# Kernel tuning notes

Hardware: AMD Instinct MI355X
Metric: run time of the kernel (lower is better)

Reference implementation:

```python
import jax, jax.numpy as jnp
import numpy as np

B, N, DIM = 2, 4096, 1024
HEADS, HEAD_DIM, CHUNK, LAYERS, HID = 16, 64, 128, 4, 4096
SCALE = HEAD_DIM ** -0.5
EPS = 1e-6


def _bitlinear(x, w, b):
    # BitLinear 1.58b: ternary weights + int8 activations with STE
    w_scale = jnp.maximum(jnp.mean(jnp.abs(w)), 1e-5)
    w_norm = w / w_scale
    w_q = w_norm + jax.lax.stop_gradient(jnp.sign(w_norm) - w_norm)
    x_scale = jnp.maximum(jnp.max(jnp.abs(x), axis=-1, keepdims=True), 1e-5)
    x_norm = x / x_scale * 127.0
    x_q = x_norm + jax.lax.stop_gradient(jnp.round(x_norm) - x_norm)
    out = (x_q @ w_q.T) * (x_scale * w_scale / 127.0)
    return out + b


def _rmsnorm(x, w):
    return x * jax.lax.rsqrt(jnp.mean(x * x, axis=-1, keepdims=True) + EPS) * w


def _rope_tables(n, d):
    inv = 1.0 / (10000.0 ** (jnp.arange(0, d, 2, dtype=jnp.float32) / d))
    f = jnp.arange(n, dtype=jnp.float32)[:, None] * inv[None, :]  # (N, d/2)
    return jnp.cos(f), jnp.sin(f)


def _apply_rope(x, cos, sin):
    # x: (B,N,H,D); complex pairs are consecutive last-dim elements
    xr, xi = x[..., 0::2], x[..., 1::2]
    c = cos[None, :, None, :]
    s = sin[None, :, None, :]
    or_ = xr * c - xi * s
    oi_ = xr * s + xi * c
    return jnp.stack([or_, oi_], axis=-1).reshape(x.shape)


def _attention(x, qkv_w, qkv_b, gate_w, gate_b, proj_w, proj_b, norm_w, cos, sin):
    b, n, c = x.shape
    qkv = _bitlinear(x, qkv_w, qkv_b).reshape(b, n, 3, HEADS, HEAD_DIM)
    q, k, v = qkv[:, :, 0], qkv[:, :, 1], qkv[:, :, 2]
    q = _apply_rope(q, cos, sin)
    k = _apply_rope(k, cos, sin)
    g = jax.nn.sigmoid(_bitlinear(x, gate_w, gate_b)).reshape(b, n, HEADS, HEAD_DIM)
    nc = n // CHUNK  # N is a multiple of CHUNK, so no padding

    def chunked(t):  # (B,N,H,D) -> (nc,B,L,H,D)
        return t.reshape(b, nc, CHUNK, HEADS, HEAD_DIM).transpose(1, 0, 2, 3, 4)

    def step(kv, inp):
        qi, ki, vi, gi = inp  # (B,L,H,D)
        # NOTE: faithful to source — attention mixes over the HEAD axis per position
        attn = jax.nn.softmax(jnp.einsum('blhd,blgd->blhg', qi, ki) * SCALE, axis=-1)
        out = jnp.einsum('blhg,blgd->blhd', attn, vi) + jnp.einsum('blhd,bhde->blhe', qi, kv)
        decay = jnp.mean(gi, axis=1)[..., None]  # (B,H,D,1)
        kv = kv * decay + jnp.einsum('blhd,blhe->bhde', ki, vi)
        return kv, out

    kv0 = jnp.zeros((b, HEADS, HEAD_DIM, HEAD_DIM), x.dtype)
    _, outs = jax.lax.scan(step, kv0, (chunked(q), chunked(k), chunked(v), chunked(g)))
    out = outs.transpose(1, 0, 2, 3, 4).reshape(b, n, c)
    return _bitlinear(_rmsnorm(out, norm_w), proj_w, proj_b)


def _mlp(x, fc1_w, fc1_b, fc2_w, fc2_b):
    h = _bitlinear(x, fc1_w, fc1_b)
    a, gate = jnp.split(h, 2, axis=-1)
    return _bitlinear(a * jax.nn.silu(gate), fc2_w, fc2_b)


def setup_inputs() -> dict:
    key = jax.random.key(0)
    ks = jax.random.split(key, 12)
    s = 0.02
    return {
        'x': jax.random.normal(ks[0], (B, N, DIM), jnp.float32),
        'norm1_w': jnp.ones((LAYERS, DIM), jnp.float32),
        'qkv_w': s * jax.random.normal(ks[1], (LAYERS, 3 * DIM, DIM), jnp.float32),
        'qkv_b': 0.01 * jax.random.normal(ks[2], (LAYERS, 3 * DIM), jnp.float32),
        'gate_w': s * jax.random.normal(ks[3], (LAYERS, DIM, DIM), jnp.float32),
        'gate_b': 0.01 * jax.random.normal(ks[4], (LAYERS, DIM), jnp.float32),
        'proj_w': s * jax.random.normal(ks[5], (LAYERS, DIM, DIM), jnp.float32),
        'proj_b': 0.01 * jax.random.normal(ks[6], (LAYERS, DIM), jnp.float32),
        'attn_norm_w': jnp.ones((LAYERS, DIM), jnp.float32),
        'norm2_w': jnp.ones((LAYERS, DIM), jnp.float32),
        'fc1_w': s * jax.random.normal(ks[7], (LAYERS, 2 * HID, DIM), jnp.float32),
        'fc1_b': 0.01 * jax.random.normal(ks[8], (LAYERS, 2 * HID), jnp.float32),
        'fc2_w': s * jax.random.normal(ks[9], (LAYERS, DIM, HID), jnp.float32),
        'fc2_b': 0.01 * jax.random.normal(ks[10], (LAYERS, DIM), jnp.float32),
    }


def reference(x, norm1_w, qkv_w, qkv_b, gate_w, gate_b, proj_w, proj_b,
              attn_norm_w, norm2_w, fc1_w, fc1_b, fc2_w, fc2_b):
    cos, sin = _rope_tables(x.shape[1], HEAD_DIM)
    for l in range(norm1_w.shape[0]):
        x = x + _attention(_rmsnorm(x, norm1_w[l]), qkv_w[l], qkv_b[l], gate_w[l],
                           gate_b[l], proj_w[l], proj_b[l], attn_norm_w[l], cos, sin)
        x = x + _mlp(_rmsnorm(x, norm2_w[l]), fc1_w[l], fc1_b[l], fc2_w[l], fc2_b[l])
    return x
```

## Files before the change

kernel.cpp:

```cpp
#include <hip/hip_runtime.h>
#include <hip/hip_bf16.h>
#include <cstdint>
#include <cstddef>

#define NLAYERS 4
#define SEQ     4096
#define DIMC    1024
#define CHUNKL  128
#define NCHUNK  32
#define HIDF    4096
#define NTOK    8192

using i32x4 = __attribute__((ext_vector_type(4))) int;

__device__ __forceinline__ void gload16(const void* g, void* l) {
    __builtin_amdgcn_global_load_lds((const __attribute__((address_space(1))) void*)g,
                                     (__attribute__((address_space(3))) void*)l, 16, 0, 0);
}

__device__ __forceinline__ float waveSum(float v) {
#pragma unroll
    for (int o = 32; o >= 1; o >>= 1) v += __shfl_down(v, o);
    return v;
}
__device__ __forceinline__ float waveMax(float v) {
#pragma unroll
    for (int o = 32; o >= 1; o >>= 1) v = fmaxf(v, __shfl_down(v, o));
    return v;
}

__global__ __launch_bounds__(256) void prep_k(const float* __restrict__ w, int8_t* __restrict__ q,
                                              float* __restrict__ part, int perlayer4) {
    __shared__ float red[4];
    int blk = blockIdx.x, layer = blockIdx.y, tid = threadIdx.x;
    const float4* p = (const float4*)(w + (size_t)layer * perlayer4 * 4);
    char4* qp = (char4*)(q + (size_t)layer * perlayer4 * 4);
    float s = 0.f;
    for (int i = blk * 256 + tid; i < perlayer4; i += 256 * 256) {
        float4 v = p[i];
        s += fabsf(v.x) + fabsf(v.y) + fabsf(v.z) + fabsf(v.w);
        char4 o;
        o.x = (v.x > 0.f) ? 1 : ((v.x < 0.f) ? -1 : 0);
        o.y = (v.y > 0.f) ? 1 : ((v.y < 0.f) ? -1 : 0);
        o.z = (v.z > 0.f) ? 1 : ((v.z < 0.f) ? -1 : 0);
        o.w = (v.w > 0.f) ? 1 : ((v.w < 0.f) ? -1 : 0);
        qp[i] = o;
    }
    s = waveSum(s);
    int lane = tid & 63, wv = tid >> 6;
    if (lane == 0) red[wv] = s;
    __syncthreads();
    if (tid == 0) part[layer * 256 + blk] = red[0] + red[1] + red[2] + red[3];
}

__global__ __launch_bounds__(256) void amean_fin(const float* __restrict__ part,
                                                 float* __restrict__ wsc, int perlayer) {
    __shared__ float red[4];
    int layer = blockIdx.x, tid = threadIdx.x;
    float s = part[layer * 256 + tid];
    s = waveSum(s);
    int lane = tid & 63, wv = tid >> 6;
    if (lane == 0) red[wv] = s;
    __syncthreads();
    if (tid == 0) {
        float tot = red[0] + red[1] + red[2] + red[3];
        wsc[layer] = fmaxf(tot / (float)perlayer, 1e-5f);
    }
}

__global__ __launch_bounds__(256) void ropetab_k(float* __restrict__ ct, float* __restrict__ st) {
    int i = blockIdx.x * 256 + threadIdx.x;
    int n = i >> 5, j = i & 31;
    float inv = exp2f(-(float)j * (13.287712379549449f / 32.0f));
    float f = (float)n * inv;
    ct[i] = cosf(f);
    st[i] = sinf(f);
}

__device__ __forceinline__ float4 rope4(float4 v, const float* ct, const float* st, int n, int j0) {
    float c0 = ct[n * 32 + j0], s0 = st[n * 32 + j0];
    float c1 = ct[n * 32 + j0 + 1], s1 = st[n * 32 + j0 + 1];
    float4 r;
    r.x = v.x * c0 - v.y * s0;
    r.y = v.x * s0 + v.y * c0;
    r.z = v.z * c1 - v.w * s1;
    r.w = v.z * s1 + v.w * c1;
    return r;
}

__global__ __launch_bounds__(256) void rmsq_k(const float* __restrict__ x, const float* __restrict__ w,
                                              int8_t* __restrict__ xq, float* __restrict__ xs) {
    __shared__ float red[4];
    int row = blockIdx.x, tid = threadIdx.x;
    const float4* xr = (const float4*)(x + (size_t)row * DIMC);
    float4 v = xr[tid];
    float ss = v.x * v.x + v.y * v.y + v.z * v.z + v.w * v.w;
    ss = waveSum(ss);
    int lane = tid & 63, wv = tid >> 6;
    if (lane == 0) red[wv] = ss;
    __syncthreads();
    float tot = red[0] + red[1] + red[2] + red[3];
    __syncthreads();
    float rinv = 1.0f / sqrtf(tot * (1.0f / (float)DIMC) + 1e-6f);
    float4 wv4 = ((const float4*)w)[tid];
    float4 y;
    y.x = v.x * rinv * wv4.x; y.y = v.y * rinv * wv4.y;
    y.z = v.z * rinv * wv4.z; y.w = v.w * rinv * wv4.w;
    float mx = fmaxf(fmaxf(fabsf(y.x), fabsf(y.y)), fmaxf(fabsf(y.z), fabsf(y.w)));
    mx = waveMax(mx);
    if (lane == 0) red[wv] = mx;
    __syncthreads();
    float s = fmaxf(fmaxf(fmaxf(red[0], red[1]), fmaxf(red[2], red[3])), 1e-5f);
    if (tid == 0) xs[row] = s;
    float qf = 127.0f / s;
    char4 o;
    o.x = (signed char)(int)rintf(y.x * qf);
    o.y = (signed char)(int)rintf(y.y * qf);
    o.z = (signed char)(int)rintf(y.z * qf);
    o.w = (signed char)(int)rintf(y.w * qf);
    ((char4*)xq)[(size_t)row * 256 + tid] = o;
}

__global__ __launch_bounds__(256) void qrow_k(const float* __restrict__ in,
                                              int8_t* __restrict__ q, float* __restrict__ xs) {
    __shared__ float red[4];
    int row = blockIdx.x, tid = threadIdx.x;
    const float4* xr = (const float4*)(in + (size_t)row * HIDF);
    float4 vv[4];
    float mx = 0.f;
#pragma unroll
    for (int j = 0; j < 4; ++j) {
        vv[j] = xr[j * 256 + tid];
        mx = fmaxf(mx, fmaxf(fmaxf(fabsf(vv[j].x), fabsf(vv[j].y)), fmaxf(fabsf(vv[j].z), fabsf(vv[j].w))));
    }
    mx = waveMax(mx);
    int lane = tid & 63, wv = tid >> 6;
    if (lane == 0) red[wv] = mx;
    __syncthreads();
    float s = fmaxf(fmaxf(fmaxf(red[0], red[1]), fmaxf(red[2], red[3])), 1e-5f);
    if (tid == 0) xs[row] = s;
    float qf = 127.0f / s;
#pragma unroll
    for (int j = 0; j < 4; ++j) {
        char4 o;
        o.x = (signed char)(int)rintf(vv[j].x * qf);
        o.y = (signed char)(int)rintf(vv[j].y * qf);
        o.z = (signed char)(int)rintf(vv[j].z * qf);
        o.w = (signed char)(int)rintf(vv[j].w * qf);
        ((char4*)q)[(size_t)row * 1024 + j * 256 + tid] = o;
    }
}

#define EPI_PLAIN 0
#define EPI_RESID 2

template <int EPI>
__global__ __launch_bounds__(256, 4) void gemm_i8(const int8_t* __restrict__ A,
                                                  const int8_t* __restrict__ B,
                                                  const float* __restrict__ xs,
                                                  const float* __restrict__ wsp,
                                                  const float* __restrict__ bias,
                                                  float* __restrict__ out,
                                                  int N, int K, int ldo) {
    __shared__ __align__(16) int8_t As[16384];
    __shared__ __align__(16) int8_t Bs[16384];
    const int tid = threadIdx.x;
    const int lane = tid & 63, wave = tid >> 6;
    const int wr = wave >> 1, wc = wave & 1;
    const int bm = blockIdx.x, bn = blockIdx.y;

    const int rA = tid >> 3;
    const int colb = (((tid & 7) ^ (rA & 7)) << 4);
    const int8_t* ap = A + (size_t)(bm * 128 + rA) * K + colb;
    const int8_t* bp = B + (size_t)(bn * 128 + rA) * K + colb;
    const size_t rstep = (size_t)32 * K;

    i32x4 acc[4][4] = {};
    const int fr = lane & 15, ks = lane >> 4;

    for (int kt = 0; kt < K; kt += 128) {
#pragma unroll
        for (int p = 0; p < 4; ++p) {
            gload16(ap + kt + (size_t)p * rstep, As + p * 4096 + tid * 16);
            gload16(bp + kt + (size_t)p * rstep, Bs + p * 4096 + tid * 16);
        }
        __syncthreads();
#pragma unroll
        for (int kh = 0; kh < 2; ++kh) {
            i32x4 af[4], bf[4];
#pragma unroll
            for (int m = 0; m < 4; ++m) {
                int ra = wr * 64 + m * 16 + fr;
                af[m] = *(const i32x4*)(As + ra * 128 + (((kh * 4 + ks) ^ (ra & 7)) << 4));
            }
#pragma unroll
            for (int n = 0; n < 4; ++n) {
                int rb = wc * 64 + n * 16 + fr;
                bf[n] = *(const i32x4*)(Bs + rb * 128 + (((kh * 4 + ks) ^ (rb & 7)) << 4));
            }
#pragma unroll
            for (int m = 0; m < 4; ++m)
#pragma unroll
                for (int n = 0; n < 4; ++n)
                    acc[m][n] = __builtin_amdgcn_mfma_i32_16x16x64_i8(af[m], bf[n], acc[m][n], 0, 0, 0);
        }
        __syncthreads();
    }

    const float ws = *wsp;
#pragma unroll
    for (int m = 0; m < 4; ++m) {
        int row0 = bm * 128 + wr * 64 + m * 16 + ks * 4;
#pragma unroll
        for (int n = 0; n < 4; ++n) {
            int col = bn * 128 + wc * 64 + n * 16 + fr;
            float bv = bias[col];
#pragma unroll
            for (int j = 0; j < 4; ++j) {
                int row = row0 + j;
                float v = (float)acc[m][n][j] * (xs[row] * ws * (1.0f / 127.0f)) + bv;
                size_t idx = (size_t)row * ldo + col;
                if (EPI == EPI_PLAIN) out[idx] = v;
                else                  out[idx] += v;
            }
        }
    }
    (void)N;
}

__global__ __launch_bounds__(256, 4) void gate_decay(const int8_t* __restrict__ A,
                                                     const int8_t* __restrict__ B,
                                                     const float* __restrict__ xs,
                                                     const float* __restrict__ wsp,
                                                     const float* __restrict__ bias,
                                                     float* __restrict__ dec) {
    __shared__ __align__(16) int8_t As[16384];
    __shared__ __align__(16) int8_t Bs[16384];
    __shared__ float dsum[2][128];
    const int tid = threadIdx.x;
    const int lane = tid & 63, wave = tid >> 6;
    const int wr = wave >> 1, wc = wave & 1;
    const int bm = blockIdx.x, bn = blockIdx.y;
    const int K = 1024;

    const int rA = tid >> 3;
    const int colb = (((tid & 7) ^ (rA & 7)) << 4);
    const int8_t* ap = A + (size_t)(bm * 128 + rA) * K + colb;
    const int8_t* bp = B + (size_t)(bn * 128 + rA) * K + colb;
    const size_t rstep = (size_t)32 * K;

    i32x4 acc[4][4] = {};
    const int fr = lane & 15, ks = lane >> 4;

    for (int kt = 0; kt < K; kt += 128) {
#pragma unroll
        for (int p = 0; p < 4; ++p) {
            gload16(ap + kt + (size_t)p * rstep, As + p * 4096 + tid * 16);
            gload16(bp + kt + (size_t)p * rstep, Bs + p * 4096 + tid * 16);
        }
        __syncthreads();
#pragma unroll
        for (int kh = 0; kh < 2; ++kh) {
            i32x4 af[4], bf[4];
#pragma unroll
            for (int m = 0; m < 4; ++m) {
                int ra = wr * 64 + m * 16 + fr;
                af[m] = *(const i32x4*)(As + ra * 128 + (((kh * 4 + ks) ^ (ra & 7)) << 4));
            }
#pragma unroll
            for (int n = 0; n < 4; ++n) {
                int rb = wc * 64 + n * 16 + fr;
                bf[n] = *(const i32x4*)(Bs + rb * 128 + (((kh * 4 + ks) ^ (rb & 7)) << 4));
            }
#pragma unroll
            for (int m = 0; m < 4; ++m)
#pragma unroll
                for (int n = 0; n < 4; ++n)
                    acc[m][n] = __builtin_amdgcn_mfma_i32_16x16x64_i8(af[m], bf[n], acc[m][n], 0, 0, 0);
        }
        __syncthreads();
    }

    const float ws = *wsp;
#pragma unroll
    for (int n = 0; n < 4; ++n) {
        int col = bn * 128 + wc * 64 + n * 16 + fr;
        float bv = bias[col];
        float sn = 0.f;
#pragma unroll
        for (int m = 0; m < 4; ++m) {
            int row0 = bm * 128 + wr * 64 + m * 16 + ks * 4;
#pragma unroll
            for (int j = 0; j < 4; ++j) {
                int row = row0 + j;
                float v = (float)acc[m][n][j] * (xs[row] * ws * (1.0f / 127.0f)) + bv;
                sn += 1.0f / (1.0f + expf(-v));
            }
        }
        sn += __shfl_down(sn, 32);
        sn += __shfl_down(sn, 16);
        if (lane < 16) dsum[wr][wc * 64 + n * 16 + lane] = sn;
    }
    __syncthreads();
    if (tid < 128) {
        int b = bm >> 5, c = bm & 31;
        dec[(size_t)(c * 2 + b) * 1024 + bn * 128 + tid] =
            (dsum[0][tid] + dsum[1][tid]) * (1.0f / 128.0f);
    }
}

__global__ __launch_bounds__(256, 4) void gemm_fc1(const int8_t* __restrict__ A,
                                                   const int8_t* __restrict__ B1,
                                                   const int8_t* __restrict__ B2,
                                                   const float* __restrict__ xs,
                                                   const float* __restrict__ wsp,
                                                   const float* __restrict__ bias,
                                                   float* __restrict__ out) {
    __shared__ __align__(16) int8_t As[16384];
    __shared__ __align__(16) int8_t Bs1[8192];
    __shared__ __align__(16) int8_t Bs2[8192];
    const int tid = threadIdx.x;
    const int lane = tid & 63, wave = tid >> 6;
    const int wr = wave >> 1, wc = wave & 1;
    const int bm = blockIdx.x, bn = blockIdx.y;
    const int K = 1024;

    const int rA = tid >> 3;
    const int colb = (((tid & 7) ^ (rA & 7)) << 4);
    const int8_t* ap  = A  + (size_t)(bm * 128 + rA) * K + colb;
    const int8_t* b1p = B1 + (size_t)(bn * 64 + rA) * K + colb;
    const int8_t* b2p = B2 + (size_t)(bn * 64 + rA) * K + colb;
    const size_t rstep = (size_t)32 * K;

    i32x4 acc1[4][2] = {}, acc2[4][2] = {};
    const int fr = lane & 15, ks = lane >> 4;

    for (int kt = 0; kt < K; kt += 128) {
#pragma unroll
        for (int p = 0; p < 4; ++p)
            gload16(ap + kt + (size_t)p * rstep, As + p * 4096 + tid * 16);
#pragma unroll
        for (int p = 0; p < 2; ++p) {
            gload16(b1p + kt + (size_t)p * rstep, Bs1 + p * 4096 + tid * 16);
            gload16(b2p + kt + (size_t)p * rstep, Bs2 + p * 4096 + tid * 16);
        }
        __syncthreads();
#pragma unroll
        for (int kh = 0; kh < 2; ++kh) {
            i32x4 af[4], b1f[2], b2f[2];
#pragma unroll
            for (int m = 0; m < 4; ++m) {
                int ra = wr * 64 + m * 16 + fr;
                af[m] = *(const i32x4*)(As + ra * 128 + (((kh * 4 + ks) ^ (ra & 7)) << 4));
            }
#pragma unroll
            for (int n = 0; n < 2; ++n) {
                int rb = wc * 32 + n * 16 + fr;
                int off = rb * 128 + (((kh * 4 + ks) ^ (rb & 7)) << 4);
                b1f[n] = *(const i32x4*)(Bs1 + off);
                b2f[n] = *(const i32x4*)(Bs2 + off);
            }
#pragma unroll
            for (int m = 0; m < 4; ++m)
#pragma unroll
                for (int n = 0; n < 2; ++n) {
                    acc1[m][n] = __builtin_amdgcn_mfma_i32_16x16x64_i8(af[m], b1f[n], acc1[m][n], 0, 0, 0);
                    acc2[m][n] = __builtin_amdgcn_mfma_i32_16x16x64_i8(af[m], b2f[n], acc2[m][n], 0, 0, 0);
                }
        }
        __syncthreads();
    }

    const float ws = *wsp;
#pragma unroll
    for (int m = 0; m < 4; ++m) {
        int row0 = bm * 128 + wr * 64 + m * 16 + ks * 4;
#pragma unroll
        for (int n = 0; n < 2; ++n) {
            int col = bn * 64 + wc * 32 + n * 16 + fr;
            float ba = bias[col];
            float bg = bias[col + 4096];
#pragma unroll
            for (int j = 0; j < 4; ++j) {
                int row = row0 + j;
                float sc = xs[row] * ws * (1.0f / 127.0f);
                float a = (float)acc1[m][n][j] * sc + ba;
                float g = (float)acc2[m][n][j] * sc + bg;
                out[(size_t)row * HIDF + col] = a * g / (1.0f + expf(-g));
            }
        }
    }
}

__global__ __launch_bounds__(256) void attn_intra(const float* __restrict__ qkv,
                                                  const float* __restrict__ ct,
                                                  const float* __restrict__ st,
                                                  float* __restrict__ o) {
    __shared__ float q_s[1024], k_s[1024], v_s[1024], p_s[256];
    int t = blockIdx.x, tid = threadIdx.x;
    int n = t & (SEQ - 1);
    int j0 = (tid & 15) * 2;
    const float4* src = (const float4*)(qkv + (size_t)t * 3072);
    ((float4*)q_s)[tid] = rope4(src[tid], ct, st, n, j0);
    ((float4*)k_s)[tid] = rope4(src[256 + tid], ct, st, n, j0);
    ((float4*)v_s)[tid] = src[512 + tid];
    __syncthreads();
    int h = tid >> 4, g = tid & 15;
    const float4* q4 = (const float4*)q_s + h * 16;
    const float4* k4 = (const float4*)k_s + g * 16;
    float accS = 0.f;
#pragma unroll
    for (int i = 0; i < 16; ++i) {
        float4 qa = q4[i], ka = k4[i];
        accS += qa.x * ka.x + qa.y * ka.y + qa.z * ka.z + qa.w * ka.w;
    }
    accS *= 0.125f;
    float mx = accS;
#pragma unroll
    for (int o2 = 8; o2 >= 1; o2 >>= 1) mx = fmaxf(mx, __shfl_xor(mx, o2, 16));
    float e = expf(accS - mx);
    float sm = e;
#pragma unroll
    for (int o2 = 8; o2 >= 1; o2 >>= 1) sm += __shfl_xor(sm, o2, 16);
    p_s[tid] = e / sm;
    __syncthreads();
    int dq = tid & 15;
    float4 acc = {0.f, 0.f, 0.f, 0.f};
    const float4* v4 = (const float4*)v_s;
#pragma unroll
    for (int gg = 0; gg < 16; ++gg) {
        float p = p_s[h * 16 + gg];
        float4 vv = v4[gg * 16 + dq];
        acc.x += p * vv.x; acc.y += p * vv.y; acc.z += p * vv.z; acc.w += p * vv.w;
    }
    ((float4*)(o + (size_t)t * DIMC))[h * 16 + dq] = acc;
}

__global__ __launch_bounds__(256) void u_k(const float* __restrict__ qkv,
                                           const float* __restrict__ ct,
                                           const float* __restrict__ st,
                                           float* __restrict__ U) {
    __shared__ float ks_[8192], vs_[8192];
    int bid = blockIdx.x, tid = threadIdx.x;
    int c = bid >> 5, b = (bid >> 4) & 1, h = bid & 15;
    size_t tok = (size_t)(b * SEQ + c * CHUNKL);
#pragma unroll
    for (int j = 0; j < 8; ++j) {
        int idx = j * 256 + tid;
        int l = idx >> 4, c4 = idx & 15;
        int n = (int)((tok + l) & (SEQ - 1));
        const float* kp = qkv + (tok + l) * 3072 + 1024 + h * 64 + c4 * 4;
        const float* vp = qkv + (tok + l) * 3072 + 2048 + h * 64 + c4 * 4;
        ((float4*)ks_)[idx] = rope4(*(const float4*)kp, ct, st, n, c4 * 2);
        ((float4*)vs_)[idx] = *(const float4*)vp;
    }
    __syncthreads();
    int d = tid >> 2, eg = tid & 3;
    float4 acc[4] = {};
    for (int l = 0; l < CHUNKL; ++l) {
        float kd = ks_[l * 64 + d];
        const float4* vrow = (const float4*)(vs_ + l * 64) + eg * 4;
#pragma unroll
        for (int i = 0; i < 4; ++i) {
            float4 vv = vrow[i];
            acc[i].x += kd * vv.x; acc[i].y += kd * vv.y;
            acc[i].z += kd * vv.z; acc[i].w += kd * vv.w;
        }
    }
    float4* Up = (float4*)(U + (size_t)bid * 4096) + d * 16 + eg * 4;
#pragma unroll
    for (int i = 0; i < 4; ++i) Up[i] = acc[i];
}

__global__ __launch_bounds__(256) void scan_k(const float* __restrict__ U,
                                              const float* __restrict__ dec,
                                              float* __restrict__ kvprev) {
    int t = blockIdx.x * 256 + threadIdx.x;
    int b = t >> 16;
    int h = (t >> 12) & 15;
    int d = (t >> 6) & 63;
    float val = 0.f;
#pragma unroll 1
    for (int c = 0; c < NCHUNK; ++c) {
        kvprev[(size_t)c * 131072 + t] = val;
        val = val * dec[(c * 2 + b) * 1024 + h * 64 + d] + U[(size_t)c * 131072 + t];
    }
}

__global__ __launch_bounds__(256) void out2_k(const float* __restrict__ qkv,
                                              const float* __restrict__ ct,
                                              const float* __restrict__ st,
                                              const float* __restrict__ kvprev,
                                              float* __restrict__ o) {
    __shared__ float kv_s[4096];
    __shared__ float q_s[128 * 65];
    int bid = blockIdx.x, tid = threadIdx.x;
    int c = bid >> 5, b = (bid >> 4) & 1, h = bid & 15;
    size_t tok = (size_t)(b * SEQ + c * CHUNKL);
    const float4* kvsrc = (const float4*)(kvprev + (size_t)c * 131072 + b * 65536 + h * 4096);
#pragma unroll
    for (int j = 0; j < 4; ++j) ((float4*)kv_s)[j * 256 + tid] = kvsrc[j * 256 + tid];
#pragma unroll
    for (int j = 0; j < 8; ++j) {
        int idx = j * 256 + tid;
        int l = idx >> 4, c4 = idx & 15;
        int n = (int)((tok + l) & (SEQ - 1));
        float4 qv = rope4(*(const float4*)(qkv + (tok + l) * 3072 + h * 64 + c4 * 4),
                          ct, st, n, c4 * 2);
        float* dq = q_s + l * 65 + c4 * 4;
        dq[0] = qv.x; dq[1] = qv.y; dq[2] = qv.z; dq[3] = qv.w;
    }
    __syncthreads();
    int l = tid >> 1, eh = tid & 1;
    float4 acc[8] = {};
    const float* qrow = q_s + l * 65;
    for (int d = 0; d < 64; ++d) {
        float qd = qrow[d];
        const float4* kvr = (const float4*)(kv_s + d * 64) + eh * 8;
#pragma unroll
        for (int i = 0; i < 8; ++i) {
            float4 kk = kvr[i];
            acc[i].x += qd * kk.x; acc[i].y += qd * kk.y;
            acc[i].z += qd * kk.z; acc[i].w += qd * kk.w;
        }
    }
    float4* op = (float4*)(o + (tok + l) * DIMC + h * 64 + eh * 32);
#pragma unroll
    for (int i = 0; i < 8; ++i) {
        float4 cur = op[i];
        cur.x += acc[i].x; cur.y += acc[i].y; cur.z += acc[i].z; cur.w += acc[i].w;
        op[i] = cur;
    }
}

extern "C" void kernel_launch(void* const* d_in, const int* in_sizes, int n_in,
                              void* d_out, int out_size, void* d_ws, size_t ws_size,
                              hipStream_t stream) {
    const float* x_in       = (const float*)d_in[0];
    const float* norm1_w    = (const float*)d_in[1];
    const float* qkv_w      = (const float*)d_in[2];
    const float* qkv_b      = (const float*)d_in[3];
    const float* gate_w     = (const float*)d_in[4];
    const float* gate_b     = (const float*)d_in[5];
    const float* proj_w     = (const float*)d_in[6];
    const float* proj_b     = (const float*)d_in[7];
    const float* attn_norm_w= (const float*)d_in[8];
    const float* norm2_w    = (const float*)d_in[9];
    const float* fc1_w      = (const float*)d_in[10];
    const float* fc1_b      = (const float*)d_in[11];
    const float* fc2_w      = (const float*)d_in[12];
    const float* fc2_b      = (const float*)d_in[13];
    float* x = (float*)d_out;

    char* wsb = (char*)d_ws;
    size_t off = 0;
    auto carve = [&](size_t bytes) { char* p = wsb + off; off = (off + bytes + 255) & ~(size_t)255; return p; };
    int8_t* q_qkv  = (int8_t*)carve(12582912);
    int8_t* q_gate = (int8_t*)carve(4194304);
    int8_t* q_proj = (int8_t*)carve(4194304);
    int8_t* q_fc1  = (int8_t*)carve(33554432);
    int8_t* q_fc2  = (int8_t*)carve(16777216);
    float*  wsc    = (float*)carve(256);
    float*  part   = (float*)carve(4096);
    float*  ropec  = (float*)carve(524288);
    float*  ropes  = (float*)carve(524288);
    int8_t* qbuf   = (int8_t*)carve(33554432);
    float*  xsbuf  = (float*)carve(32768);
    float*  big    = (float*)carve(134217728);
    float*  attn_o = (float*)carve(33554432);
    float*  Ub     = (float*)carve(16777216);
    float*  kvprev = (float*)carve(16777216);
    float*  decayb = (float*)carve(262144);
    (void)ws_size; (void)in_sizes; (void)n_in; (void)out_size;

    hipMemcpyAsync(x, x_in, (size_t)NTOK * DIMC * sizeof(float), hipMemcpyDeviceToDevice, stream);
    ropetab_k<<<512, 256, 0, stream>>>(ropec, ropes);

    struct WSpec { const float* w; int8_t* q; int perlayer; int arr; };
    WSpec specs[5] = {
        {qkv_w,  q_qkv,  3 * DIMC * DIMC, 0},
        {gate_w, q_gate, DIMC * DIMC,     1},
        {proj_w, q_proj, DIMC * DIMC,     2},
        {fc1_w,  q_fc1,  8192 * 1024,     3},
        {fc2_w,  q_fc2,  DIMC * HIDF,     4},
    };
    for (int a = 0; a < 5; ++a) {
        prep_k<<<dim3(256, NLAYERS), 256, 0, stream>>>(specs[a].w, specs[a].q, part, specs[a].perlayer / 4);
        amean_fin<<<NLAYERS, 256, 0, stream>>>(part, wsc + specs[a].arr * 4, specs[a].perlayer);
    }

    for (int l = 0; l < NLAYERS; ++l) {
        rmsq_k<<<NTOK, 256, 0, stream>>>(x, norm1_w + l * DIMC, qbuf, xsbuf);
        gemm_i8<EPI_PLAIN><<<dim3(64, 24), 256, 0, stream>>>(
            qbuf, q_qkv + (size_t)l * 3145728, xsbuf, wsc + 0 * 4 + l,
            qkv_b + l * 3072, big, 3072, 1024, 3072);
        gate_decay<<<dim3(64, 8), 256, 0, stream>>>(
            qbuf, q_gate + (size_t)l * 1048576, xsbuf, wsc + 1 * 4 + l,
            gate_b + l * DIMC, decayb);
        attn_intra<<<NTOK, 256, 0, stream>>>(big, ropec, ropes, attn_o);
        u_k<<<1024, 256, 0, stream>>>(big, ropec, ropes, Ub);
        scan_k<<<512, 256, 0, stream>>>(Ub, decayb, kvprev);
        out2_k<<<1024, 256, 0, stream>>>(big, ropec, ropes, kvprev, attn_o);
        rmsq_k<<<NTOK, 256, 0, stream>>>(attn_o, attn_norm_w + l * DIMC, qbuf, xsbuf);
        gemm_i8<EPI_RESID><<<dim3(64, 8), 256, 0, stream>>>(
            qbuf, q_proj + (size_t)l * 1048576, xsbuf, wsc + 2 * 4 + l,
            proj_b + l * DIMC, x, 1024, 1024, 1024);
        rmsq_k<<<NTOK, 256, 0, stream>>>(x, norm2_w + l * DIMC, qbuf, xsbuf);
        gemm_fc1<<<dim3(64, 64), 256, 0, stream>>>(
            qbuf, q_fc1 + (size_t)l * 8388608, q_fc1 + (size_t)l * 8388608 + 4194304,
            xsbuf, wsc + 3 * 4 + l, fc1_b + l * 8192, big);
        qrow_k<<<NTOK, 256, 0, stream>>>(big, qbuf, xsbuf);
        gemm_i8<EPI_RESID><<<dim3(64, 8), 256, 0, stream>>>(
            qbuf, q_fc2 + (size_t)l * 4194304, xsbuf, wsc + 4 * 4 + l,
            fc2_b + l * DIMC, x, 1024, 4096, 1024);
    }
}
```

Before: 2.008 ms.

## Double-buffer LDS tiles in int8 GEMMs to overlap loads with MFMA

Converts the three int8 MFMA GEMM kernels from a single 128-wide K tile (load, sync, compute, sync) to a double-buffered 64-wide K tile. The next tile's global->LDS loads are issued before computing on the current buffer, so memory latency can overlap with matrix math. The XOR swizzle is adjusted for 64-byte rows. It keeps the same LDS footprint but takes twice as many loop iterations, and so twice as many barriers per K. It also relies on the barrier at the end of each iteration to make the async LDS loads visible.

```diff
diff --git a/kernel.cpp b/kernel.cpp
--- a/kernel.cpp
+++ b/kernel.cpp
@@ -162,49 +162,56 @@
                                                   const float* __restrict__ bias,
                                                   float* __restrict__ out,
                                                   int N, int K, int ldo) {
-    __shared__ __align__(16) int8_t As[16384];
-    __shared__ __align__(16) int8_t Bs[16384];
+    __shared__ __align__(16) int8_t As[2][8192];
+    __shared__ __align__(16) int8_t Bs[2][8192];
     const int tid = threadIdx.x;
     const int lane = tid & 63, wave = tid >> 6;
     const int wr = wave >> 1, wc = wave & 1;
     const int bm = blockIdx.x, bn = blockIdx.y;
 
-    const int rA = tid >> 3;
-    const int colb = (((tid & 7) ^ (rA & 7)) << 4);
-    const int8_t* ap = A + (size_t)(bm * 128 + rA) * K + colb;
-    const int8_t* bp = B + (size_t)(bn * 128 + rA) * K + colb;
-    const size_t rstep = (size_t)32 * K;
+    const int r0 = tid >> 2, sl = tid & 3;
+    const int c0 = ((sl ^ ((r0 >> 1) & 3)) << 4);
+    const int r1 = r0 + 64;
+    const int8_t* a0 = A + (size_t)(bm * 128 + r0) * K + c0;
+    const int8_t* a1 = A + (size_t)(bm * 128 + r1) * K + c0;
+    const int8_t* b0 = B + (size_t)(bn * 128 + r0) * K + c0;
+    const int8_t* b1 = B + (size_t)(bn * 128 + r1) * K + c0;
 
     i32x4 acc[4][4] = {};
     const int fr = lane & 15, ks = lane >> 4;
 
-    for (int kt = 0; kt < K; kt += 128) {
-#pragma unroll
-        for (int p = 0; p < 4; ++p) {
-            gload16(ap + kt + (size_t)p * rstep, As + p * 4096 + tid * 16);
-            gload16(bp + kt + (size_t)p * rstep, Bs + p * 4096 + tid * 16);
-        }
+    gload16(a0, As[0] + tid * 16);
+    gload16(a1, As[0] + 4096 + tid * 16);
+    gload16(b0, Bs[0] + tid * 16);
+    gload16(b1, Bs[0] + 4096 + tid * 16);
+    __syncthreads();
+
+    int cur = 0;
+    for (int kt = 0; kt < K; kt += 64) {
+        if (kt + 64 < K) {
+            gload16(a0 + kt + 64, As[cur ^ 1] + tid * 16);
+            gload16(a1 + kt + 64, As[cur ^ 1] + 4096 + tid * 16);
+            gload16(b0 + kt + 64, Bs[cur ^ 1] + tid * 16);
+            gload16(b1 + kt + 64, Bs[cur ^ 1] + 4096 + tid * 16);
+        }
+        i32x4 af[4], bf[4];
+#pragma unroll
+        for (int m = 0; m < 4; ++m) {
+            int ra = wr * 64 + m * 16 + fr;
+            af[m] = *(const i32x4*)(As[cur] + ra * 64 + ((ks ^ ((ra >> 1) & 3)) << 4));
+        }
+#pragma unroll
+        for (int n = 0; n < 4; ++n) {
+            int rb = wc * 64 + n * 16 + fr;
+            bf[n] = *(const i32x4*)(Bs[cur] + rb * 64 + ((ks ^ ((rb >> 1) & 3)) << 4));
+        }
+#pragma unroll
+        for (int m = 0; m < 4; ++m)
+#pragma unroll
+            for (int n = 0; n < 4; ++n)
+                acc[m][n] = __builtin_amdgcn_mfma_i32_16x16x64_i8(af[m], bf[n], acc[m][n], 0, 0, 0);
         __syncthreads();
-#pragma unroll
-        for (int kh = 0; kh < 2; ++kh) {
-            i32x4 af[4], bf[4];
-#pragma unroll
-            for (int m = 0; m < 4; ++m) {
-                int ra = wr * 64 + m * 16 + fr;
-                af[m] = *(const i32x4*)(As + ra * 128 + (((kh * 4 + ks) ^ (ra & 7)) << 4));
-            }
-#pragma unroll
-            for (int n = 0; n < 4; ++n) {
-                int rb = wc * 64 + n * 16 + fr;
-                bf[n] = *(const i32x4*)(Bs + rb * 128 + (((kh * 4 + ks) ^ (rb & 7)) << 4));
-            }
-#pragma unroll
-            for (int m = 0; m < 4; ++m)
-#pragma unroll
-                for (int n = 0; n < 4; ++n)
-                    acc[m][n] = __builtin_amdgcn_mfma_i32_16x16x64_i8(af[m], bf[n], acc[m][n], 0, 0, 0);
-        }
-        __syncthreads();
+        cur ^= 1;
     }
 
     const float ws = *wsp;
@@ -234,8 +241,8 @@
                                                      const float* __restrict__ wsp,
                                                      const float* __restrict__ bias,
                                                      float* __restrict__ dec) {
-    __shared__ __align__(16) int8_t As[16384];
-    __shared__ __align__(16) int8_t Bs[16384];
+    __shared__ __align__(16) int8_t As[2][8192];
+    __shared__ __align__(16) int8_t Bs[2][8192];
     __shared__ float dsum[2][128];
     const int tid = threadIdx.x;
     const int lane = tid & 63, wave = tid >> 6;
@@ -243,42 +250,49 @@
     const int bm = blockIdx.x, bn = blockIdx.y;
     const int K = 1024;
 
-    const int rA = tid >> 3;
-    const int colb = (((tid & 7) ^ (rA & 7)) << 4);
-    const int8_t* ap = A + (size_t)(bm * 128 + rA) * K + colb;
-    const int8_t* bp = B + (size_t)(bn * 128 + rA) * K + colb;
-    const size_t rstep = (size_t)32 * K;
+    const int r0 = tid >> 2, sl = tid & 3;
+    const int c0 = ((sl ^ ((r0 >> 1) & 3)) << 4);
+    const int r1 = r0 + 64;
+    const int8_t* a0 = A + (size_t)(bm * 128 + r0) * K + c0;
+    const int8_t* a1 = A + (size_t)(bm * 128 + r1) * K + c0;
+    const int8_t* b0 = B + (size_t)(bn * 128 + r0) * K + c0;
+    const int8_t* b1 = B + (size_t)(bn * 128 + r1) * K + c0;
 
     i32x4 acc[4][4] = {};
     const int fr = lane & 15, ks = lane >> 4;
 
-    for (int kt = 0; kt < K; kt += 128) {
-#pragma unroll
-        for (int p = 0; p < 4; ++p) {
-            gload16(ap + kt + (size_t)p * rstep, As + p * 4096 + tid * 16);
-            gload16(bp + kt + (size_t)p * rstep, Bs + p * 4096 + tid * 16);
-        }
+    gload16(a0, As[0] + tid * 16);
+    gload16(a1, As[0] + 4096 + tid * 16);
+    gload16(b0, Bs[0] + tid * 16);
+    gload16(b1, Bs[0] + 4096 + tid * 16);
+    __syncthreads();
+
+    int cur = 0;
+    for (int kt = 0; kt < K; kt += 64) {
+        if (kt + 64 < K) {
+            gload16(a0 + kt + 64, As[cur ^ 1] + tid * 16);
+            gload16(a1 + kt + 64, As[cur ^ 1] + 4096 + tid * 16);
+            gload16(b0 + kt + 64, Bs[cur ^ 1] + tid * 16);
+            gload16(b1 + kt + 64, Bs[cur ^ 1] + 4096 + tid * 16);
+        }
+        i32x4 af[4], bf[4];
+#pragma unroll
+        for (int m = 0; m < 4; ++m) {
+            int ra = wr * 64 + m * 16 + fr;
+            af[m] = *(const i32x4*)(As[cur] + ra * 64 + ((ks ^ ((ra >> 1) & 3)) << 4));
+        }
+#pragma unroll
+        for (int n = 0; n < 4; ++n) {
+            int rb = wc * 64 + n * 16 + fr;
+            bf[n] = *(const i32x4*)(Bs[cur] + rb * 64 + ((ks ^ ((rb >> 1) & 3)) << 4));
+        }
+#pragma unroll
+        for (int m = 0; m < 4; ++m)
+#pragma unroll
+            for (int n = 0; n < 4; ++n)
+                acc[m][n] = __builtin_amdgcn_mfma_i32_16x16x64_i8(af[m], bf[n], acc[m][n], 0, 0, 0);
         __syncthreads();
-#pragma unroll
-        for (int kh = 0; kh < 2; ++kh) {
-            i32x4 af[4], bf[4];
-#pragma unroll
-            for (int m = 0; m < 4; ++m) {
-                int ra = wr * 64 + m * 16 + fr;
-                af[m] = *(const i32x4*)(As + ra * 128 + (((kh * 4 + ks) ^ (ra & 7)) << 4));
-            }
-#pragma unroll
-            for (int n = 0; n < 4; ++n) {
-                int rb = wc * 64 + n * 16 + fr;
-                bf[n] = *(const i32x4*)(Bs + rb * 128 + (((kh * 4 + ks) ^ (rb & 7)) << 4));
-            }
-#pragma unroll
-            for (int m = 0; m < 4; ++m)
-#pragma unroll
-                for (int n = 0; n < 4; ++n)
-                    acc[m][n] = __builtin_amdgcn_mfma_i32_16x16x64_i8(af[m], bf[n], acc[m][n], 0, 0, 0);
-        }
-        __syncthreads();
+        cur ^= 1;
     }
 
     const float ws = *wsp;
@@ -316,59 +330,62 @@
                                                    const float* __restrict__ wsp,
                                                    const float* __restrict__ bias,
                                                    float* __restrict__ out) {
-    __shared__ __align__(16) int8_t As[16384];
-    __shared__ __align__(16) int8_t Bs1[8192];
-    __shared__ __align__(16) int8_t Bs2[8192];
+    __shared__ __align__(16) int8_t As[2][8192];
+    __shared__ __align__(16) int8_t Bs1[2][4096];
+    __shared__ __align__(16) int8_t Bs2[2][4096];
     const int tid = threadIdx.x;
     const int lane = tid & 63, wave = tid >> 6;
     const int wr = wave >> 1, wc = wave & 1;
     const int bm = blockIdx.x, bn = blockIdx.y;
     const int K = 1024;
 
-    const int rA = tid >> 3;
-    const int colb = (((tid & 7) ^ (rA & 7)) << 4);
-    const int8_t* ap  = A  + (size_t)(bm * 128 + rA) * K + colb;
-    const int8_t* b1p = B1 + (size_t)(bn * 64 + rA) * K + colb;
-    const int8_t* b2p = B2 + (size_t)(bn * 64 + rA) * K + colb;
-    const size_t rstep = (size_t)32 * K;
+    const int r0 = tid >> 2, sl = tid & 3;
+    const int c0 = ((sl ^ ((r0 >> 1) & 3)) << 4);
+    const int r1 = r0 + 64;
+    const int8_t* a0  = A  + (size_t)(bm * 128 + r0) * K + c0;
+    const int8_t* a1  = A  + (size_t)(bm * 128 + r1) * K + c0;
+    const int8_t* b1p = B1 + (size_t)(bn * 64 + r0) * K + c0;
+    const int8_t* b2p = B2 + (size_t)(bn * 64 + r0) * K + c0;
 
     i32x4 acc1[4][2] = {}, acc2[4][2] = {};
     const int fr = lane & 15, ks = lane >> 4;
 
-    for (int kt = 0; kt < K; kt += 128) {
-#pragma unroll
-        for (int p = 0; p < 4; ++p)
-            gload16(ap + kt + (size_t)p * rstep, As + p * 4096 + tid * 16);
-#pragma unroll
-        for (int p = 0; p < 2; ++p) {
-            gload16(b1p + kt + (size_t)p * rstep, Bs1 + p * 4096 + tid * 16);
-            gload16(b2p + kt + (size_t)p * rstep, Bs2 + p * 4096 + tid * 16);
-        }
+    gload16(a0,  As[0] + tid * 16);
+    gload16(a1,  As[0] + 4096 + tid * 16);
+    gload16(b1p, Bs1[0] + tid * 16);
+    gload16(b2p, Bs2[0] + tid * 16);
+    __syncthreads();
+
+    int cur = 0;
+    for (int kt = 0; kt < K; kt += 64) {
+        if (kt + 64 < K) {
+            gload16(a0  + kt + 64, As[cur ^ 1] + tid * 16);
+            gload16(a1  + kt + 64, As[cur ^ 1] + 4096 + tid * 16);
+            gload16(b1p + kt + 64, Bs1[cur ^ 1] + tid * 16);
+            gload16(b2p + kt + 64, Bs2[cur ^ 1] + tid * 16);
+        }
+        i32x4 af[4], b1f[2], b2f[2];
+#pragma unroll
+        for (int m = 0; m < 4; ++m) {
+            int ra = wr * 64 + m * 16 + fr;
+            af[m] = *(const i32x4*)(As[cur] + ra * 64 + ((ks ^ ((ra >> 1) & 3)) << 4));
+        }
+#pragma unroll
+        for (int n = 0; n < 2; ++n) {
+            int rb = wc * 32 + n * 16 + fr;
+            int off = rb * 64 + ((ks ^ ((rb >> 1) & 3)) << 4);
+            b1f[n] = *(const i32x4*)(Bs1[cur] + off);
+            b2f[n] = *(const i32x4*)(Bs2[cur] + off);
+        }
+#pragma unroll
+        for (int m = 0; m < 4; ++m)
+#pragma unroll
+            for (int n = 0; n < 2; ++n) {
+                acc1[m][n] = __builtin_amdgcn_mfma_i32_16x16x64_i8(af[m], b1f[n], acc1[m][n], 0, 0, 0);
+                acc2[m][n] = __builtin_amdgcn_mfma_i32_16x16x64_i8(af[m], b2f[n], acc2[m][n], 0, 0, 0);
+            }
         __syncthreads();
-#pragma unroll
-        for (int kh = 0; kh < 2; ++kh) {
-            i32x4 af[4], b1f[2], b2f[2];
-#pragma unroll
-            for (int m = 0; m < 4; ++m) {
-                int ra = wr * 64 + m * 16 + fr;
-                af[m] = *(const i32x4*)(As + ra * 128 + (((kh * 4 + ks) ^ (ra & 7)) << 4));
-            }
-#pragma unroll
-            for (int n = 0; n < 2; ++n) {
-                int rb = wc * 32 + n * 16 + fr;
-                int off = rb * 128 + (((kh * 4 + ks) ^ (rb & 7)) << 4);
-                b1f[n] = *(const i32x4*)(Bs1 + off);
-                b2f[n] = *(const i32x4*)(Bs2 + off);
-            }
-#pragma unroll
-            for (int m = 0; m < 4; ++m)
-#pragma unroll
-                for (int n = 0; n < 2; ++n) {
-                    acc1[m][n] = __builtin_amdgcn_mfma_i32_16x16x64_i8(af[m], b1f[n], acc1[m][n], 0, 0, 0);
-                    acc2[m][n] = __builtin_amdgcn_mfma_i32_16x16x64_i8(af[m], b2f[n], acc2[m][n], 0, 0, 0);
-                }
-        }
-        __syncthreads();
+        cur ^= 1;
     }
 
     const float ws = *wsp;
```

New measurement: 2.146 ms. 6.9% more time.

## Double-buffer fc1 int8 GEMM K-loop with async LDS prefetch

Applied to the files above, without the earlier changes.

Restructures the gated fc1 int8 GEMM main loop into a two-stage pipeline. K tiles shrink from 128 to 64 and are double-buffered in LDS, with the load for tile t+2 issued right after the current tile's fragments are read into registers. Explicit vmcnt/lgkmcnt waits and raw barriers replace the full __syncthreads pairs. The goal is to hide global-to-LDS load latency behind the MFMA work. In exchange the loop runs twice as many iterations with smaller tiles, and the swizzle changes to fit 64-byte rows.

```diff
diff --git a/kernel.cpp b/kernel.cpp
--- a/kernel.cpp
+++ b/kernel.cpp
@@ -316,60 +316,68 @@
                                                    const float* __restrict__ wsp,
                                                    const float* __restrict__ bias,
                                                    float* __restrict__ out) {
-    __shared__ __align__(16) int8_t As[16384];
-    __shared__ __align__(16) int8_t Bs1[8192];
-    __shared__ __align__(16) int8_t Bs2[8192];
+    __shared__ __align__(16) int8_t As[2][8192];
+    __shared__ __align__(16) int8_t Bs1[2][4096];
+    __shared__ __align__(16) int8_t Bs2[2][4096];
     const int tid = threadIdx.x;
     const int lane = tid & 63, wave = tid >> 6;
     const int wr = wave >> 1, wc = wave & 1;
     const int bm = blockIdx.x, bn = blockIdx.y;
     const int K = 1024;
 
-    const int rA = tid >> 3;
-    const int colb = (((tid & 7) ^ (rA & 7)) << 4);
-    const int8_t* ap  = A  + (size_t)(bm * 128 + rA) * K + colb;
-    const int8_t* b1p = B1 + (size_t)(bn * 64 + rA) * K + colb;
-    const int8_t* b2p = B2 + (size_t)(bn * 64 + rA) * K + colb;
-    const size_t rstep = (size_t)32 * K;
+    const int r0 = tid >> 2, sl = tid & 3;
+    const int c0 = ((sl ^ ((r0 >> 1) & 3)) << 4);
+    const int r1 = r0 + 64;
+    const int8_t* a0  = A  + (size_t)(bm * 128 + r0) * K + c0;
+    const int8_t* a1  = A  + (size_t)(bm * 128 + r1) * K + c0;
+    const int8_t* b1p = B1 + (size_t)(bn * 64 + r0) * K + c0;
+    const int8_t* b2p = B2 + (size_t)(bn * 64 + r0) * K + c0;
 
     i32x4 acc1[4][2] = {}, acc2[4][2] = {};
     const int fr = lane & 15, ks = lane >> 4;
 
-    for (int kt = 0; kt < K; kt += 128) {
-#pragma unroll
-        for (int p = 0; p < 4; ++p)
-            gload16(ap + kt + (size_t)p * rstep, As + p * 4096 + tid * 16);
-#pragma unroll
-        for (int p = 0; p < 2; ++p) {
-            gload16(b1p + kt + (size_t)p * rstep, Bs1 + p * 4096 + tid * 16);
-            gload16(b2p + kt + (size_t)p * rstep, Bs2 + p * 4096 + tid * 16);
-        }
-        __syncthreads();
-#pragma unroll
-        for (int kh = 0; kh < 2; ++kh) {
-            i32x4 af[4], b1f[2], b2f[2];
-#pragma unroll
-            for (int m = 0; m < 4; ++m) {
-                int ra = wr * 64 + m * 16 + fr;
-                af[m] = *(const i32x4*)(As + ra * 128 + (((kh * 4 + ks) ^ (ra & 7)) << 4));
-            }
+#define STAGE_FC1(buf, kt_)  do {                         \
+        gload16(a0  + (kt_), As[buf] + tid * 16);         \
+        gload16(a1  + (kt_), As[buf] + 4096 + tid * 16);  \
+        gload16(b1p + (kt_), Bs1[buf] + tid * 16);        \
+        gload16(b2p + (kt_), Bs2[buf] + tid * 16);        \
+    } while (0)
+
+    STAGE_FC1(0, 0);
+    STAGE_FC1(1, 64);
+
+    const int NT = 16;
+    for (int t = 0; t < NT; ++t) {
+        const int cur = t & 1;
+        if (t < NT - 1) asm volatile("s_waitcnt vmcnt(4)" ::: "memory");
+        else            asm volatile("s_waitcnt vmcnt(0)" ::: "memory");
+        __builtin_amdgcn_s_barrier();
+        i32x4 af[4], b1f[2], b2f[2];
+#pragma unroll
+        for (int m = 0; m < 4; ++m) {
+            int ra = wr * 64 + m * 16 + fr;
+            af[m] = *(const i32x4*)(As[cur] + ra * 64 + ((ks ^ ((ra >> 1) & 3)) << 4));
+        }
+#pragma unroll
+        for (int n = 0; n < 2; ++n) {
+            int rb = wc * 32 + n * 16 + fr;
+            int off = rb * 64 + ((ks ^ ((rb >> 1) & 3)) << 4);
+            b1f[n] = *(const i32x4*)(Bs1[cur] + off);
+            b2f[n] = *(const i32x4*)(Bs2[cur] + off);
+        }
+        asm volatile("s_waitcnt lgkmcnt(0)" ::: "memory");
+        __builtin_amdgcn_s_barrier();
+        __builtin_amdgcn_sched_barrier(0);
+        if (t + 2 < NT) STAGE_FC1(cur, (t + 2) * 64);
+#pragma unroll
+        for (int m = 0; m < 4; ++m)
 #pragma unroll
             for (int n = 0; n < 2; ++n) {
-                int rb = wc * 32 + n * 16 + fr;
-                int off = rb * 128 + (((kh * 4 + ks) ^ (rb & 7)) << 4);
-                b1f[n] = *(const i32x4*)(Bs1 + off);
-                b2f[n] = *(const i32x4*)(Bs2 + off);
-            }
-#pragma unroll
-            for (int m = 0; m < 4; ++m)
-#pragma unroll
-                for (int n = 0; n < 2; ++n) {
-                    acc1[m][n] = __builtin_amdgcn_mfma_i32_16x16x64_i8(af[m], b1f[n], acc1[m][n], 0, 0, 0);
-                    acc2[m][n] = __builtin_amdgcn_mfma_i32_16x16x64_i8(af[m], b2f[n], acc2[m][n], 0, 0, 0);
-                }
-        }
-        __syncthreads();
-    }
+                acc1[m][n] = __builtin_amdgcn_mfma_i32_16x16x64_i8(af[m], b1f[n], acc1[m][n], 0, 0, 0);
+                acc2[m][n] = __builtin_amdgcn_mfma_i32_16x16x64_i8(af[m], b2f[n], acc2[m][n], 0, 0, 0);
+            }
+    }
+#undef STAGE_FC1
 
     const float ws = *wsp;
 #pragma unroll
```

After: 2.024 ms. About the same (+0.8%).
